# Kernel optimization log

Hardware: AMD Instinct MI355X
Metric: run time of the kernel (lower is better)

The kernel has to match this reference:

```python
import jax, jax.numpy as jnp
import numpy as np

DIM = 768
EPS = 1e-06


def _layernorm(x, gamma, beta):
    # LayerNorm over last axis (channels), eps=EPS, elementwise affine
    mu = jnp.mean(x, axis=-1, keepdims=True)
    var = jnp.mean(jnp.square(x - mu), axis=-1, keepdims=True)
    return (x - mu) * jax.lax.rsqrt(var + EPS) * gamma + beta


def setup_inputs() -> dict:
    key = jax.random.key(0)
    ks = jax.random.split(key, 10)
    B, C, H, W = 16, DIM, 32, 32
    s = 1.0 / np.sqrt(C)  # mimic Conv2d default init scale
    return {
        "x": jax.random.normal(ks[0], (B, C, H, W), dtype=jnp.float32),
        "W1": jax.random.uniform(ks[1], (C, C), jnp.float32, -s, s),
        "b1": jax.random.uniform(ks[2], (C,), jnp.float32, -s, s),
        "g1": jnp.ones((C,), jnp.float32),
        "beta1": jnp.zeros((C,), jnp.float32),
        "W2": jax.random.uniform(ks[3], (C, C), jnp.float32, -s, s),
        "b2": jax.random.uniform(ks[4], (C,), jnp.float32, -s, s),
        "g2": jnp.ones((C,), jnp.float32),
        "beta2": jnp.zeros((C,), jnp.float32),
        "W3": jax.random.uniform(ks[5], (C, C), jnp.float32, -s, s),
        "b3": jax.random.uniform(ks[6], (C,), jnp.float32, -s, s),
    }


def reference(x, W1, b1, g1, beta1, W2, b2, g2, beta2, W3, b3):
    # x: [B, C, H, W] (NCHW). Work in NHWC; 1x1 conv == channel matmul.
    h = jnp.transpose(x, (0, 2, 3, 1))  # [B, H, W, C]
    h = jnp.einsum("bhwc,oc->bhwo", h, W1) + b1
    h = jax.nn.gelu(_layernorm(h, g1, beta1), approximate=False)
    h = jnp.einsum("bhwc,oc->bhwo", h, W2) + b2
    h = jax.nn.gelu(_layernorm(h, g2, beta2), approximate=False)
    h = jnp.einsum("bhwc,oc->bhwo", h, W3) + b3
    return jnp.transpose(h, (0, 3, 1, 2))  # back to NCHW
```

## Files before the change

### kernel.cpp

```cpp
#include <hip/hip_runtime.h>
#include <hip/hip_bf16.h>

typedef __bf16 bf16;
typedef __bf16 bf16x4 __attribute__((ext_vector_type(4)));
typedef __bf16 bf16x8 __attribute__((ext_vector_type(8)));
typedef float f32x4 __attribute__((ext_vector_type(4)));

#define DIM 768
#define HW 1024
#define BATCH 16
#define M_TOTAL (BATCH * HW)
#define NKT 12

#define AS1 __attribute__((address_space(1)))
#define AS3 __attribute__((address_space(3)))


__global__ void prep_kernel(const float* __restrict__ x, bf16* __restrict__ xb,
                            const float4* __restrict__ w1, const float4* __restrict__ w2,
                            const float4* __restrict__ w3,
                            bf16x8* __restrict__ o1, bf16x8* __restrict__ o2,
                            bf16x8* __restrict__ o3) {
    __shared__ float tile[32][33];
    if (blockIdx.x < 864) {
        const int b = blockIdx.x;
        const int which = b / 288;
        const int i = (b % 288) * 256 + threadIdx.x;
        const float4* w = which == 0 ? w1 : which == 1 ? w2 : w3;
        bf16x8* o = which == 0 ? o1 : which == 1 ? o2 : o3;
        const int row = i / 96, br = i % 96;
        const int q = br >> 2, g = br & 3;
        float4 lo = w[row * 192 + q * 8 + g];
        float4 hi = w[row * 192 + q * 8 + g + 4];
        bf16x8 r = { (bf16)lo.x, (bf16)lo.y, (bf16)lo.z, (bf16)lo.w,
                     (bf16)hi.x, (bf16)hi.y, (bf16)hi.z, (bf16)hi.w };
        o[row * 96 + br] = r;
    } else {
        const int e = blockIdx.x - 864;
        const int b = e / 768;
        const int rem = e % 768;
        const int c0 = (rem / 32) * 32;
        const int hw0 = (rem % 32) * 32;
        const int tx = threadIdx.x & 31, ty = threadIdx.x >> 5;

        const float* src = x + ((size_t)b * DIM + c0) * HW + hw0;
#pragma unroll
        for (int j = 0; j < 4; j++)
            tile[ty + 8 * j][tx] = src[(size_t)(ty + 8 * j) * HW + tx];
        __syncthreads();
        const int ptx = (((tx & 15) >> 2) << 3) + (tx & 3) + ((tx >> 4) << 2);
        bf16* dst = xb + ((size_t)b * HW + hw0) * DIM + c0;
#pragma unroll
        for (int j = 0; j < 4; j++)
            dst[(size_t)(ty + 8 * j) * DIM + ptx] = (bf16)tile[tx][ty + 8 * j];
    }
}

template <int MODE>
__global__ __launch_bounds__(256, 2) void gemm_kernel(
    const bf16* __restrict__ A,
    const bf16* __restrict__ Bw,
    const float* __restrict__ bias,
    void* __restrict__ out)
{
    constexpr int K = DIM;
    __shared__ bf16 ldsA[2][128][64];
    __shared__ bf16 ldsB[2][192][64];

    const int t = threadIdx.x;
    const int lane = t & 63;
    const int wave = t >> 6;
    const int wm = wave >> 1, wn = wave & 1;

    const int bid = blockIdx.x;
    const int virt = (bid & 7) * 64 + (bid >> 3);
    const int m0 = (virt >> 2) * 128;
    const int n0 = (virt & 3) * 192;

    const int fr = lane & 15;
    const int fq = lane >> 4;

    f32x4 acc[4][6] = {};

    const int s_r = t >> 3;
    const int s_blk = t & 7;

    auto stage_chunk = [&](int kt, int c) {
        const int d = kt & 1;
#pragma unroll
        for (int j = 0; j < 2; j++) {
            const int rr = s_r + j * 32;
            if (c < 2) {
                const int r = c * 64 + rr;
                __builtin_amdgcn_global_load_lds(
                    (const AS1 void*)(A + (size_t)(m0 + r) * K + kt * 64 + ((s_blk ^ (r & 7)) << 3)),
                    (AS3 void*)&ldsA[d][r][s_blk * 8], 16, 0, 0);
            } else {
                const int r = (c - 2) * 64 + rr;
                __builtin_amdgcn_global_load_lds(
                    (const AS1 void*)(Bw + (size_t)(n0 + r) * K + kt * 64 + ((s_blk ^ (r & 7)) << 3)),
                    (AS3 void*)&ldsB[d][r][s_blk * 8], 16, 0, 0);
            }
        }
    };

    bf16x8 a[8], b[12];

    auto ldA = [&](int kt) {
        const int d = kt & 1;
#pragma unroll
        for (int mi = 0; mi < 4; mi++) {
            const int R = wm * 64 + mi * 16 + fr;
            const bf16* rp = &ldsA[d][R][0];
            const int s = R & 7;
#pragma unroll
            for (int ks = 0; ks < 2; ks++)
                a[mi * 2 + ks] = *(const bf16x8*)(rp + (((ks * 4 + fq) ^ s) << 3));
        }
    };
    auto ldB = [&](int kt) {
        const int d = kt & 1;
#pragma unroll
        for (int j = 0; j < 6; j++) {
            const int R = wn * 96 + j * 16 + fr;
            const bf16* rp = &ldsB[d][R][0];
            const int s = R & 7;
#pragma unroll
            for (int ks = 0; ks < 2; ks++)
                b[j * 2 + ks] = *(const bf16x8*)(rp + (((ks * 4 + fq) ^ s) << 3));
        }
    };
    auto MM = [&](int j0, int j1) {
        __builtin_amdgcn_s_setprio(1);
#pragma unroll
        for (int mi = 0; mi < 4; mi++)
#pragma unroll
            for (int j = 0; j < 6; j++)
                if (j >= j0 && j < j1)
#pragma unroll
                    for (int ks = 0; ks < 2; ks++)
                        acc[mi][j] = __builtin_amdgcn_mfma_f32_16x16x32_bf16(
                            a[mi * 2 + ks], b[j * 2 + ks], acc[mi][j], 0, 0, 0);
        __builtin_amdgcn_s_setprio(0);
    };

#pragma unroll
    for (int c = 0; c < 5; c++) stage_chunk(0, c);
    stage_chunk(1, 0); stage_chunk(1, 1);
    asm volatile("s_waitcnt vmcnt(4)" ::: "memory");
    __builtin_amdgcn_s_barrier();

    for (int kt = 0; kt < NKT; ++kt) {
        ldA(kt);
        ldB(kt);
        if (kt + 1 < NKT) { stage_chunk(kt + 1, 2); stage_chunk(kt + 1, 3); stage_chunk(kt + 1, 4); }
        MM(0, 4);

        asm volatile("s_waitcnt lgkmcnt(0)" ::: "memory");
        __builtin_amdgcn_s_barrier();
        if (kt + 2 < NKT) { stage_chunk(kt + 2, 0); stage_chunk(kt + 2, 1); }
        MM(4, 6);

        if (kt < NKT - 2) {
            asm volatile("s_waitcnt vmcnt(4)" ::: "memory");
            __builtin_amdgcn_s_barrier();
        } else if (kt == NKT - 2) {
            asm volatile("s_waitcnt vmcnt(0)" ::: "memory");
            __builtin_amdgcn_s_barrier();
        }
        __builtin_amdgcn_sched_barrier(0);
    }

    const int fq4 = fq * 4;
    if (MODE == 0) {
        bf16* o = (bf16*)out;
#pragma unroll
        for (int mi = 0; mi < 4; mi++) {
            const int row = m0 + wm * 64 + mi * 16 + fq4;
#pragma unroll
            for (int j = 0; j < 6; j++) {
                const int gcol = n0 + wn * 96 + j * 16 + fr;
                const int kk = gcol & 31;
                const int pcol = (gcol & ~31) + (((kk & 15) >> 2) << 3) + (kk & 3)
                               + ((kk >> 4) << 2);
                const float bv = bias[gcol];
#pragma unroll
                for (int r = 0; r < 4; r++)
                    o[(size_t)(row + r) * DIM + pcol] = (bf16)(acc[mi][j][r] + bv);
            }
        }
    } else {
        float* o = (float*)out;
#pragma unroll
        for (int mi = 0; mi < 4; mi++) {
            const int nb = m0 + wm * 64 + mi * 16 + fq4;
            const int bI = nb >> 10, hw = nb & 1023;
#pragma unroll
            for (int j = 0; j < 6; j++) {
                const int col = n0 + wn * 96 + j * 16 + fr;
                f32x4 v = acc[mi][j] + bias[col];
                *(f32x4*)(o + ((size_t)bI * DIM + col) * HW + hw) = v;
            }
        }
    }
}

__global__ __launch_bounds__(256) void ln_gelu_kernel(
    bf16* __restrict__ h, const float* __restrict__ g, const float* __restrict__ beta)
{
    const int wave = threadIdx.x >> 6;
    const int lane = threadIdx.x & 63;
    const int n = blockIdx.x * 4 + wave;
    bf16* row = h + (size_t)n * DIM;

    float v[12];
    float s = 0.f, ss = 0.f;
#pragma unroll
    for (int j = 0; j < 3; j++) {
        bf16x4 x = *(const bf16x4*)(row + j * 256 + lane * 4);
#pragma unroll
        for (int i = 0; i < 4; i++) {
            float f = (float)x[i];
            v[j * 4 + i] = f;
            s += f;
            ss += f * f;
        }
    }
#pragma unroll
    for (int off = 32; off > 0; off >>= 1) {
        s += __shfl_xor(s, off);
        ss += __shfl_xor(ss, off);
    }
    const float mu = s * (1.f / DIM);
    const float var = ss * (1.f / DIM) - mu * mu;
    const float rstd = rsqrtf(var + 1e-6f);

#pragma unroll
    for (int j = 0; j < 3; j++) {
        bf16x4 r;
#pragma unroll
        for (int i = 0; i < 4; i++) {
            const int c = j * 256 + lane * 4 + i;
            const int p = (lane * 4 + i) & 31;
            const int kk = ((p >> 3) << 2) + (p & 7) + ((p & 4) ? 12 : 0);
            const int gi = (c & ~31) + kk;
            float y = (v[j * 4 + i] - mu) * rstd * g[gi] + beta[gi];
            y = 0.5f * y * (1.f + erff(y * 0.70710678118f));
            r[i] = (bf16)y;
        }
        *(bf16x4*)(row + j * 256 + lane * 4) = r;
    }
}

extern "C" void kernel_launch(void* const* d_in, const int* in_sizes, int n_in,
                              void* d_out, int out_size, void* d_ws, size_t ws_size,
                              hipStream_t stream) {
    const float* x   = (const float*)d_in[0];
    const float* W1  = (const float*)d_in[1];
    const float* b1  = (const float*)d_in[2];
    const float* g1  = (const float*)d_in[3];
    const float* be1 = (const float*)d_in[4];
    const float* W2  = (const float*)d_in[5];
    const float* b2  = (const float*)d_in[6];
    const float* g2  = (const float*)d_in[7];
    const float* be2 = (const float*)d_in[8];
    const float* W3  = (const float*)d_in[9];
    const float* b3  = (const float*)d_in[10];
    float* out = (float*)d_out;

    bf16* Wb1  = (bf16*)d_ws;
    bf16* Wb2  = Wb1 + (size_t)DIM * DIM;
    bf16* Wb3  = Wb2 + (size_t)DIM * DIM;
    bf16* buf0 = Wb3 + (size_t)DIM * DIM;
    bf16* buf1 = buf0 + (size_t)M_TOTAL * DIM;

    prep_kernel<<<864 + 12288, 256, 0, stream>>>(
        x, buf0, (const float4*)W1, (const float4*)W2, (const float4*)W3,
        (bf16x8*)Wb1, (bf16x8*)Wb2, (bf16x8*)Wb3);

    const int ggrid = (M_TOTAL / 128) * (DIM / 192);
    gemm_kernel<0><<<ggrid, 256, 0, stream>>>(buf0, Wb1, b1, buf1);
    ln_gelu_kernel<<<M_TOTAL / 4, 256, 0, stream>>>(buf1, g1, be1);
    gemm_kernel<0><<<ggrid, 256, 0, stream>>>(buf1, Wb2, b2, buf0);
    ln_gelu_kernel<<<M_TOTAL / 4, 256, 0, stream>>>(buf0, g2, be2);
    gemm_kernel<1><<<ggrid, 256, 0, stream>>>(buf0, Wb3, b3, out);
}
```

Measured before the change: 140.8 us.

## Load GEMM A operand directly from global into double-buffered registers, bypassing LDS

The A tile is no longer staged through shared memory. Each wave now loads its MFMA A fragments straight from global memory into two alternating register sets, relying on the pre-permuted column layout written by the previous stage. Only B still goes through double-buffered LDS, and the k-loop drops to one barrier per step. This cuts LDS footprint and barrier count, but the two N-waves now each fetch the same A rows from global/L2, and register pressure rises.

```diff
diff --git a/kernel.cpp b/kernel.cpp
--- a/kernel.cpp
+++ b/kernel.cpp
@@ -64,7 +64,6 @@
     void* __restrict__ out)
 {
     constexpr int K = DIM;
-    __shared__ bf16 ldsA[2][128][64];
     __shared__ bf16 ldsB[2][192][64];
 
     const int t = threadIdx.x;
@@ -85,39 +84,26 @@
     const int s_r = t >> 3;
     const int s_blk = t & 7;
 
-    auto stage_chunk = [&](int kt, int c) {
+    auto stageB = [&](int kt, int c) {
         const int d = kt & 1;
 #pragma unroll
         for (int j = 0; j < 2; j++) {
-            const int rr = s_r + j * 32;
-            if (c < 2) {
-                const int r = c * 64 + rr;
-                __builtin_amdgcn_global_load_lds(
-                    (const AS1 void*)(A + (size_t)(m0 + r) * K + kt * 64 + ((s_blk ^ (r & 7)) << 3)),
-                    (AS3 void*)&ldsA[d][r][s_blk * 8], 16, 0, 0);
-            } else {
-                const int r = (c - 2) * 64 + rr;
-                __builtin_amdgcn_global_load_lds(
-                    (const AS1 void*)(Bw + (size_t)(n0 + r) * K + kt * 64 + ((s_blk ^ (r & 7)) << 3)),
-                    (AS3 void*)&ldsB[d][r][s_blk * 8], 16, 0, 0);
-            }
-        }
-    };
-
-    bf16x8 a[8], b[12];
-
-    auto ldA = [&](int kt) {
-        const int d = kt & 1;
-#pragma unroll
-        for (int mi = 0; mi < 4; mi++) {
-            const int R = wm * 64 + mi * 16 + fr;
-            const bf16* rp = &ldsA[d][R][0];
-            const int s = R & 7;
-#pragma unroll
-            for (int ks = 0; ks < 2; ks++)
-                a[mi * 2 + ks] = *(const bf16x8*)(rp + (((ks * 4 + fq) ^ s) << 3));
-        }
-    };
+            const int r = c * 64 + s_r + j * 32;
+            __builtin_amdgcn_global_load_lds(
+                (const AS1 void*)(Bw + (size_t)(n0 + r) * K + kt * 64 + ((s_blk ^ (r & 7)) << 3)),
+                (AS3 void*)&ldsB[d][r][s_blk * 8], 16, 0, 0);
+        }
+    };
+
+    const int aBase = (m0 + wm * 64 + fr) * K + fq * 8;
+
+    bf16x8 aP[8], aQ[8], b[12];
+
+#define LDA(dst, kt) do { \
+    _Pragma("unroll") for (int mi = 0; mi < 4; mi++) \
+    _Pragma("unroll") for (int ks = 0; ks < 2; ks++) \
+        dst[mi * 2 + ks] = *(const bf16x8*)(A + aBase + mi * 16 * K + (kt) * 64 + ks * 32); } while (0)
+
     auto ldB = [&](int kt) {
         const int d = kt & 1;
 #pragma unroll
@@ -130,46 +116,44 @@
                 b[j * 2 + ks] = *(const bf16x8*)(rp + (((ks * 4 + fq) ^ s) << 3));
         }
     };
-    auto MM = [&](int j0, int j1) {
+    auto MM = [&](const bf16x8* src) {
         __builtin_amdgcn_s_setprio(1);
 #pragma unroll
         for (int mi = 0; mi < 4; mi++)
 #pragma unroll
             for (int j = 0; j < 6; j++)
-                if (j >= j0 && j < j1)
-#pragma unroll
-                    for (int ks = 0; ks < 2; ks++)
-                        acc[mi][j] = __builtin_amdgcn_mfma_f32_16x16x32_bf16(
-                            a[mi * 2 + ks], b[j * 2 + ks], acc[mi][j], 0, 0, 0);
+#pragma unroll
+                for (int ks = 0; ks < 2; ks++)
+                    acc[mi][j] = __builtin_amdgcn_mfma_f32_16x16x32_bf16(
+                        src[mi * 2 + ks], b[j * 2 + ks], acc[mi][j], 0, 0, 0);
         __builtin_amdgcn_s_setprio(0);
     };
 
-#pragma unroll
-    for (int c = 0; c < 5; c++) stage_chunk(0, c);
-    stage_chunk(1, 0); stage_chunk(1, 1);
-    asm volatile("s_waitcnt vmcnt(4)" ::: "memory");
+    auto body = [&](int kt, const bf16x8* cur, bf16x8* nxt) {
+        const bool more = (kt + 1 < NKT);
+        if (more) { stageB(kt + 1, 0); stageB(kt + 1, 1); stageB(kt + 1, 2); }
+        if (more) { LDA(nxt, kt + 1); }
+        ldB(kt);
+        MM(cur);
+        if (more) {
+            asm volatile("s_waitcnt lgkmcnt(0)" ::: "memory");
+            asm volatile("s_waitcnt vmcnt(8)" ::: "memory");
+            __builtin_amdgcn_s_barrier();
+            __builtin_amdgcn_sched_barrier(0);
+        }
+    };
+
+    stageB(0, 0); stageB(0, 1); stageB(0, 2);
+    LDA(aP, 0);
+    asm volatile("s_waitcnt vmcnt(8)" ::: "memory");
     __builtin_amdgcn_s_barrier();
 
-    for (int kt = 0; kt < NKT; ++kt) {
-        ldA(kt);
-        ldB(kt);
-        if (kt + 1 < NKT) { stage_chunk(kt + 1, 2); stage_chunk(kt + 1, 3); stage_chunk(kt + 1, 4); }
-        MM(0, 4);
-
-        asm volatile("s_waitcnt lgkmcnt(0)" ::: "memory");
-        __builtin_amdgcn_s_barrier();
-        if (kt + 2 < NKT) { stage_chunk(kt + 2, 0); stage_chunk(kt + 2, 1); }
-        MM(4, 6);
-
-        if (kt < NKT - 2) {
-            asm volatile("s_waitcnt vmcnt(4)" ::: "memory");
-            __builtin_amdgcn_s_barrier();
-        } else if (kt == NKT - 2) {
-            asm volatile("s_waitcnt vmcnt(0)" ::: "memory");
-            __builtin_amdgcn_s_barrier();
-        }
-        __builtin_amdgcn_sched_barrier(0);
-    }
+#pragma unroll 1
+    for (int kt2 = 0; kt2 < NKT; kt2 += 2) {
+        body(kt2, aP, aQ);
+        body(kt2 + 1, aQ, aP);
+    }
+#undef LDA
 
     const int fq4 = fq * 4;
     if (MODE == 0) {
```

After: 179.9 us. 1.28x slower.
